# Kernel optimization log

Hardware: AMD Instinct MI355X
Metric: run time of the kernel (lower is better)

The kernel has to match this reference:

```python
import jax, jax.numpy as jnp
import numpy as np
from functools import partial

# CUBA LIF/LI constants (mock-mode software integration, hxtorch conventions)
DT = 1e-6
TAU_MEM_INV = 1.0 / 6e-6   # dt*tau_mem_inv = 1/6 per-step membrane coupling
TAU_SYN_INV = 1.0 / 6e-6   # dt*tau_syn_inv = 1/6 per-step synaptic decay
ALPHA = 50.0               # SuperSpike surrogate steepness
V_TH = 1.0                 # threshold; leak = reset = 0


@partial(jax.custom_vjp, nondiff_argnums=(1,))
def spike_fn(x, alpha):
    # Heaviside forward, SuperSpike surrogate backward.
    return (x > 0.0).astype(x.dtype)

def _spike_fwd(x, alpha):
    return spike_fn(x, alpha), x

def _spike_bwd(alpha, x, g):
    return (g / (alpha * jnp.abs(x) + 1.0) ** 2,)

spike_fn.defvjp(_spike_fwd, _spike_bwd)


def cuba_lif(inp):
    """CUBA LIF integration over time. inp: [T, B, N] synaptic input; returns spikes [T, B, N]."""
    B, N = inp.shape[1], inp.shape[2]
    v0 = jnp.zeros((B, N), inp.dtype)
    i0 = jnp.zeros((B, N), inp.dtype)

    def step(carry, x):
        v, i = carry
        v = v + DT * TAU_MEM_INV * (-v + i)          # membrane update (leak=0)
        i = i * (1.0 - DT * TAU_SYN_INV) + x          # synaptic current decay + input
        z = spike_fn(v - V_TH, ALPHA)                 # spike
        v = (1.0 - jax.lax.stop_gradient(z)) * v      # reset to 0 (detached spike)
        return (v, i), z

    _, z = jax.lax.scan(step, (v0, i0), inp)
    return z


def cuba_li(inp):
    """CUBA LI (non-spiking readout) integration. inp: [T, B, N]; returns membrane trace [T, B, N]."""
    B, N = inp.shape[1], inp.shape[2]
    v0 = jnp.zeros((B, N), inp.dtype)
    i0 = jnp.zeros((B, N), inp.dtype)

    def step(carry, x):
        v, i = carry
        v = v + DT * TAU_MEM_INV * (-v + i)
        i = i * (1.0 - DT * TAU_SYN_INV) + x
        return (v, i), v

    _, v = jax.lax.scan(step, (v0, i0), inp)
    return v


def setup_inputs() -> dict:
    key = jax.random.key(0)
    k1, k2, k3 = jax.random.split(key, 3)
    T, B, N_IN, N_HID, N_OUT = 256, 128, 784, 512, 128
    spikes = (jax.random.uniform(k1, (T, B, N_IN)) < 0.1).astype(jnp.float32)
    w_hidden = 0.2 * jax.random.normal(k2, (N_HID, N_IN), dtype=jnp.float32)
    w_out = 0.2 * jax.random.normal(k3, (N_OUT, N_HID), dtype=jnp.float32)
    return {"spikes": spikes, "w_hidden": w_hidden, "w_out": w_out}


def reference(spikes, w_hidden, w_out):
    # input_repetitions=1 -> repeat is a no-op. Synapses have no bias.
    c_h = jnp.einsum('tbi,hi->tbh', spikes, w_hidden)   # [T, B, n_hidden]
    s_h = cuba_lif(c_h)                                  # hidden spikes
    c_o = jnp.einsum('tbh,oh->tbo', s_h, w_out)          # [T, B, n_out]
    return cuba_li(c_o)                                  # readout membrane trace (v_cadc)
```

## Files before the change

kernel.cpp:

```cpp
#include <hip/hip_runtime.h>

typedef _Float16 f16;
typedef _Float16 f16x8 __attribute__((ext_vector_type(8)));
typedef float f32x4 __attribute__((ext_vector_type(4)));

#define GLOBAL_AS __attribute__((address_space(1)))
#define LDS_AS __attribute__((address_space(3)))

__device__ __forceinline__ void async16(const void* g, void* l) {
  __builtin_amdgcn_global_load_lds((const GLOBAL_AS unsigned int*)g,
                                   (LDS_AS unsigned int*)l, 16, 0, 0);
}

__global__ __launch_bounds__(256) void conv_all(const float* __restrict__ s,
                                                const float* __restrict__ wh,
                                                f16* __restrict__ a16,
                                                f16* __restrict__ w2h) {
  if (blockIdx.x < 12800) {
    int idx = blockIdx.x * 256 + threadIdx.x;
    int m = idx / 100;
    int g = idx - m * 100;
    f16x8 h = {};
    if (g < 98) {
      const float4* p = (const float4*)(s + (size_t)m * 784 + g * 8);
      float4 x = p[0];
      float4 y = p[1];
      h[0] = (f16)x.x; h[1] = (f16)x.y; h[2] = (f16)x.z; h[3] = (f16)x.w;
      h[4] = (f16)y.x; h[5] = (f16)y.y; h[6] = (f16)y.z; h[7] = (f16)y.w;
    }
    *(f16x8*)(a16 + (size_t)m * 800 + g * 8) = h;
  } else {
    int idx = (blockIdx.x - 12800) * 256 + threadIdx.x;
    if (idx < 819200) {
      int h = idx / 1600;
      int c = idx - h * 1600;
      f16 o = (f16)0.f;
      if (c < 784) {
        o = (f16)wh[h * 784 + c];
      } else if (c >= 800 && c < 1584) {
        float x = wh[h * 784 + (c - 800)];
        f16 hi = (f16)x;
        o = (f16)((x - (float)hi) * 2048.0f);
      }
      w2h[idx] = o;
    }
  }
}

template <typename OUT, int N_LD, int A_STRIDE, int B_STRIDE, int NCH64,
          bool TAIL32, int B_OFF_LO, int KSPLIT_SPAN, bool XCD_SWZ>
__global__ __launch_bounds__(256, 2) void gemm_f16(const f16* __restrict__ A,
                                                   const f16* __restrict__ B,
                                                   OUT* __restrict__ C) {
  constexpr bool HAS_LO = (B_OFF_LO > 0);
  __shared__ __align__(16) f16 lds_a[128 * 64];
  __shared__ __align__(16) f16 lds_bh[128 * 64];
  __shared__ __align__(16) f16 lds_bl[HAS_LO ? 128 * 64 : 8];
  const int t = threadIdx.x;
  const int lane = t & 63;
  const int wave = t >> 6;
  int bx, by;
  if (XCD_SWZ) {
    const int b = blockIdx.x;
    by = (b & 7) + 8 * (b >> 5);
    bx = (b >> 3) & 3;
  } else {
    bx = blockIdx.x;
    by = blockIdx.y;
  }
  const int m0 = by * 128;
  const int n0 = KSPLIT_SPAN ? 0 : bx * 128;
  const int kb = KSPLIT_SPAN ? bx * KSPLIT_SPAN : 0;
  OUT* Cp = KSPLIT_SPAN ? C + (size_t)bx * 32768 * N_LD : C;
  const int wm = (wave >> 1) * 64;
  const int wn = (wave & 1) * 64;
  const int row = lane & 15;
  const int quad = lane >> 4;

  f32x4 acch[4][4] = {};
  f32x4 accl[HAS_LO ? 4 : 1][4] = {};

  for (int c = 0; c < NCH64; ++c) {
    const int k0 = kb + c * 64;
#pragma unroll
    for (int s = 0; s < 4; ++s) {
      const int j = t + s * 256;
      const int r = j >> 3;
      const int g = (j & 7) ^ (r & 7);
      async16(A + (m0 + r) * A_STRIDE + k0 + g * 8, &lds_a[j * 8]);
      async16(B + (n0 + r) * B_STRIDE + k0 + g * 8, &lds_bh[j * 8]);
      if (HAS_LO)
        async16(B + (n0 + r) * B_STRIDE + B_OFF_LO + k0 + g * 8, &lds_bl[j * 8]);
    }
    __syncthreads();
#pragma unroll
    for (int ks = 0; ks < 2; ++ks) {
      f16x8 af[4], bh[4], bl[4];
#pragma unroll
      for (int tm = 0; tm < 4; ++tm) {
        const int ra = wm + tm * 16 + row;
        const int p = (ks * 4 + quad) ^ (ra & 7);
        af[tm] = *(const f16x8*)&lds_a[ra * 64 + p * 8];
      }
#pragma unroll
      for (int tn = 0; tn < 4; ++tn) {
        const int rb = wn + tn * 16 + row;
        const int p = (ks * 4 + quad) ^ (rb & 7);
        bh[tn] = *(const f16x8*)&lds_bh[rb * 64 + p * 8];
        if (HAS_LO) bl[tn] = *(const f16x8*)&lds_bl[rb * 64 + p * 8];
      }
#pragma unroll
      for (int tm = 0; tm < 4; ++tm)
#pragma unroll
        for (int tn = 0; tn < 4; ++tn) {
          acch[tm][tn] =
              __builtin_amdgcn_mfma_f32_16x16x32_f16(af[tm], bh[tn], acch[tm][tn], 0, 0, 0);
          if (HAS_LO)
            accl[tm][tn] =
                __builtin_amdgcn_mfma_f32_16x16x32_f16(af[tm], bl[tn], accl[tm][tn], 0, 0, 0);
        }
    }
    __syncthreads();
  }

  if (TAIL32) {
    const int k0 = kb + NCH64 * 64;
#pragma unroll
    for (int s = 0; s < 2; ++s) {
      const int j = t + s * 256;
      const int r = j >> 2;
      const int g = (j & 3) ^ (r & 3);
      async16(A + (m0 + r) * A_STRIDE + k0 + g * 8, &lds_a[j * 8]);
      async16(B + (n0 + r) * B_STRIDE + k0 + g * 8, &lds_bh[j * 8]);
      if (HAS_LO)
        async16(B + (n0 + r) * B_STRIDE + B_OFF_LO + k0 + g * 8, &lds_bl[j * 8]);
    }
    __syncthreads();
    f16x8 af[4], bh[4], bl[4];
#pragma unroll
    for (int tm = 0; tm < 4; ++tm) {
      const int ra = wm + tm * 16 + row;
      const int p = quad ^ (ra & 3);
      af[tm] = *(const f16x8*)&lds_a[ra * 32 + p * 8];
    }
#pragma unroll
    for (int tn = 0; tn < 4; ++tn) {
      const int rb = wn + tn * 16 + row;
      const int p = quad ^ (rb & 3);
      bh[tn] = *(const f16x8*)&lds_bh[rb * 32 + p * 8];
      if (HAS_LO) bl[tn] = *(const f16x8*)&lds_bl[rb * 32 + p * 8];
    }
#pragma unroll
    for (int tm = 0; tm < 4; ++tm)
#pragma unroll
      for (int tn = 0; tn < 4; ++tn) {
        acch[tm][tn] =
            __builtin_amdgcn_mfma_f32_16x16x32_f16(af[tm], bh[tn], acch[tm][tn], 0, 0, 0);
        if (HAS_LO)
          accl[tm][tn] =
              __builtin_amdgcn_mfma_f32_16x16x32_f16(af[tm], bl[tn], accl[tm][tn], 0, 0, 0);
      }
  }

#pragma unroll
  for (int tm = 0; tm < 4; ++tm)
#pragma unroll
    for (int tn = 0; tn < 4; ++tn)
#pragma unroll
      for (int r = 0; r < 4; ++r) {
        const int mm = m0 + wm + tm * 16 + quad * 4 + r;
        const int nn = n0 + wn + tn * 16 + row;
        float val = acch[tm][tn][r];
        if (HAS_LO) val += 4.8828125e-4f * accl[tm][tn][r];
        Cp[(size_t)mm * N_LD + nn] = (OUT)val;
      }
}

__global__ __launch_bounds__(512, 2) void fused_bgl(const f16* __restrict__ ch,
                                                    const float* __restrict__ wo,
                                                    float* __restrict__ out) {
  const int b = blockIdx.x;
  const int tid = threadIdx.x;
  const int lane = tid & 63;
  const int wave = tid >> 6;
  const int trow = lane & 15;
  const int quad = lane >> 4;

  __shared__ __align__(16) f16 s_lds[32 * 512];
  __shared__ __align__(16) float co_lds[32][132];

  f16x8 bfrag[16];
  {
    const float* wp = wo + (wave * 16 + trow) * 512 + quad * 8;
#pragma unroll
    for (int ks = 0; ks < 16; ++ks) {
      const float4* p = (const float4*)(wp + ks * 32);
      float4 x = p[0];
      float4 y = p[1];
      f16x8 hh;
      hh[0] = (f16)x.x; hh[1] = (f16)x.y; hh[2] = (f16)x.z; hh[3] = (f16)x.w;
      hh[4] = (f16)y.x; hh[5] = (f16)y.y; hh[6] = (f16)y.z; hh[7] = (f16)y.w;
      bfrag[ks] = hh;
    }
  }

  const int h = tid;
  float v = 0.f, cur = 0.f;
  float lv = 0.f, lcur = 0.f;

  f16 xa[32], xb[32];
#pragma unroll
  for (int j = 0; j < 32; ++j) xa[j] = ch[((size_t)(j * 128 + b)) * 512 + h];

  for (int c = 0; c < 8; ++c) {
    if (c < 7) {
#pragma unroll
      for (int j = 0; j < 32; ++j)
        xb[j] = ch[((size_t)(((c + 1) * 32 + j) * 128 + b)) * 512 + h];
    }
#pragma unroll
    for (int j = 0; j < 32; ++j) {
      float x = (float)xa[j];
      v = v + 0.16666667f * (cur - v);
      cur = 0.8333333f * cur + x;
      bool z = v > 1.0f;
      v = z ? 0.f : v;
      s_lds[j * 512 + (((h >> 3) ^ (j & 7)) << 3) + (h & 7)] = z ? (f16)1.f : (f16)0.f;
    }
#pragma unroll
    for (int j = 0; j < 32; ++j) xa[j] = xb[j];
    __syncthreads();

    f32x4 acc0 = {};
    f32x4 acc1 = {};
#pragma unroll
    for (int ks = 0; ks < 16; ++ks) {
      const int G = ks * 4 + quad;
      f16x8 a0 = *(const f16x8*)&s_lds[trow * 512 + ((G ^ (trow & 7)) << 3)];
      f16x8 a1 = *(const f16x8*)&s_lds[(16 + trow) * 512 + ((G ^ (trow & 7)) << 3)];
      acc0 = __builtin_amdgcn_mfma_f32_16x16x32_f16(a0, bfrag[ks], acc0, 0, 0, 0);
      acc1 = __builtin_amdgcn_mfma_f32_16x16x32_f16(a1, bfrag[ks], acc1, 0, 0, 0);
    }
#pragma unroll
    for (int r = 0; r < 4; ++r) {
      co_lds[quad * 4 + r][wave * 16 + trow] = acc0[r];
      co_lds[16 + quad * 4 + r][wave * 16 + trow] = acc1[r];
    }
    __syncthreads();

    if (tid < 128) {
#pragma unroll
      for (int j = 0; j < 32; ++j) {
        float x = co_lds[j][tid];
        lv = lv + 0.16666667f * (lcur - lv);
        lcur = 0.8333333f * lcur + x;
        out[((size_t)((c * 32 + j) * 128 + b)) * 128 + tid] = lv;
      }
    }
  }
}

extern "C" void kernel_launch(void* const* d_in, const int* in_sizes, int n_in,
                              void* d_out, int out_size, void* d_ws, size_t ws_size,
                              hipStream_t stream) {
  const float* spikes = (const float*)d_in[0];
  const float* w_hidden = (const float*)d_in[1];
  const float* w_out = (const float*)d_in[2];
  float* out = (float*)d_out;

  char* ws = (char*)d_ws;
  f16* A16 = (f16*)ws;
  f16* w2h = (f16*)(ws + 52428800);
  f16* c_h = (f16*)(ws + 52428800 + 1638400);

  conv_all<<<16000, 256, 0, stream>>>(spikes, w_hidden, A16, w2h);

  gemm_f16<f16, 512, 800, 1600, 12, true, 800, 0, true>
      <<<1024, 256, 0, stream>>>(A16, w2h, c_h);

  fused_bgl<<<128, 512, 0, stream>>>(c_h, w_out, out);
}
```

Before: 239.3 us.

## Double-buffer GEMM1 LDS loads with async prefetch of next K chunk

Replaces the templated single-buffered GEMM with a specialized kernel that stages K in 32-wide chunks into two LDS buffers. It prefetches the next chunk with global_load_lds while computing the current one, using vmcnt waits and raw barriers. The aim is to hide global-load latency behind MFMA work. In exchange, the K step per barrier halves, so twice as many barriers run. The last iteration also issues a redundant reload of chunk 24.

```diff
diff --git a/kernel.cpp b/kernel.cpp
--- a/kernel.cpp
+++ b/kernel.cpp
@@ -47,108 +47,67 @@
   }
 }
 
-template <typename OUT, int N_LD, int A_STRIDE, int B_STRIDE, int NCH64,
-          bool TAIL32, int B_OFF_LO, int KSPLIT_SPAN, bool XCD_SWZ>
-__global__ __launch_bounds__(256, 2) void gemm_f16(const f16* __restrict__ A,
-                                                   const f16* __restrict__ B,
-                                                   OUT* __restrict__ C) {
-  constexpr bool HAS_LO = (B_OFF_LO > 0);
-  __shared__ __align__(16) f16 lds_a[128 * 64];
-  __shared__ __align__(16) f16 lds_bh[128 * 64];
-  __shared__ __align__(16) f16 lds_bl[HAS_LO ? 128 * 64 : 8];
+__global__ __launch_bounds__(256, 2) void gemm1_pipe(const f16* __restrict__ A,
+                                                     const f16* __restrict__ B,
+                                                     f16* __restrict__ C) {
+  __shared__ __align__(16) f16 lds_a[2][128 * 32];
+  __shared__ __align__(16) f16 lds_bh[2][128 * 32];
+  __shared__ __align__(16) f16 lds_bl[2][128 * 32];
   const int t = threadIdx.x;
   const int lane = t & 63;
   const int wave = t >> 6;
-  int bx, by;
-  if (XCD_SWZ) {
-    const int b = blockIdx.x;
-    by = (b & 7) + 8 * (b >> 5);
-    bx = (b >> 3) & 3;
-  } else {
-    bx = blockIdx.x;
-    by = blockIdx.y;
-  }
+  const int b = blockIdx.x;
+  const int by = (b & 7) + 8 * (b >> 5);
+  const int bx = (b >> 3) & 3;
   const int m0 = by * 128;
-  const int n0 = KSPLIT_SPAN ? 0 : bx * 128;
-  const int kb = KSPLIT_SPAN ? bx * KSPLIT_SPAN : 0;
-  OUT* Cp = KSPLIT_SPAN ? C + (size_t)bx * 32768 * N_LD : C;
+  const int n0 = bx * 128;
   const int wm = (wave >> 1) * 64;
   const int wn = (wave & 1) * 64;
   const int row = lane & 15;
   const int quad = lane >> 4;
 
+  const int j0 = t, j1 = t + 256;
+  const int r0 = j0 >> 2, g0 = (j0 & 3) ^ (r0 & 3);
+  const int r1 = j1 >> 2, g1 = (j1 & 3) ^ (r1 & 3);
+
   f32x4 acch[4][4] = {};
-  f32x4 accl[HAS_LO ? 4 : 1][4] = {};
-
-  for (int c = 0; c < NCH64; ++c) {
-    const int k0 = kb + c * 64;
-#pragma unroll
-    for (int s = 0; s < 4; ++s) {
-      const int j = t + s * 256;
-      const int r = j >> 3;
-      const int g = (j & 7) ^ (r & 7);
-      async16(A + (m0 + r) * A_STRIDE + k0 + g * 8, &lds_a[j * 8]);
-      async16(B + (n0 + r) * B_STRIDE + k0 + g * 8, &lds_bh[j * 8]);
-      if (HAS_LO)
-        async16(B + (n0 + r) * B_STRIDE + B_OFF_LO + k0 + g * 8, &lds_bl[j * 8]);
-    }
-    __syncthreads();
-#pragma unroll
-    for (int ks = 0; ks < 2; ++ks) {
-      f16x8 af[4], bh[4], bl[4];
-#pragma unroll
-      for (int tm = 0; tm < 4; ++tm) {
-        const int ra = wm + tm * 16 + row;
-        const int p = (ks * 4 + quad) ^ (ra & 7);
-        af[tm] = *(const f16x8*)&lds_a[ra * 64 + p * 8];
-      }
-#pragma unroll
-      for (int tn = 0; tn < 4; ++tn) {
-        const int rb = wn + tn * 16 + row;
-        const int p = (ks * 4 + quad) ^ (rb & 7);
-        bh[tn] = *(const f16x8*)&lds_bh[rb * 64 + p * 8];
-        if (HAS_LO) bl[tn] = *(const f16x8*)&lds_bl[rb * 64 + p * 8];
-      }
-#pragma unroll
-      for (int tm = 0; tm < 4; ++tm)
-#pragma unroll
-        for (int tn = 0; tn < 4; ++tn) {
-          acch[tm][tn] =
-              __builtin_amdgcn_mfma_f32_16x16x32_f16(af[tm], bh[tn], acch[tm][tn], 0, 0, 0);
-          if (HAS_LO)
-            accl[tm][tn] =
-                __builtin_amdgcn_mfma_f32_16x16x32_f16(af[tm], bl[tn], accl[tm][tn], 0, 0, 0);
-        }
-    }
-    __syncthreads();
-  }
-
-  if (TAIL32) {
-    const int k0 = kb + NCH64 * 64;
-#pragma unroll
-    for (int s = 0; s < 2; ++s) {
-      const int j = t + s * 256;
-      const int r = j >> 2;
-      const int g = (j & 3) ^ (r & 3);
-      async16(A + (m0 + r) * A_STRIDE + k0 + g * 8, &lds_a[j * 8]);
-      async16(B + (n0 + r) * B_STRIDE + k0 + g * 8, &lds_bh[j * 8]);
-      if (HAS_LO)
-        async16(B + (n0 + r) * B_STRIDE + B_OFF_LO + k0 + g * 8, &lds_bl[j * 8]);
-    }
-    __syncthreads();
+  f32x4 accl[4][4] = {};
+
+#define STAGE1(c, bi)                                                   \
+  {                                                                     \
+    const int k0 = (c) * 32;                                            \
+    async16(A + (m0 + r0) * 800 + k0 + g0 * 8, &lds_a[bi][j0 * 8]);     \
+    async16(A + (m0 + r1) * 800 + k0 + g1 * 8, &lds_a[bi][j1 * 8]);     \
+    async16(B + (n0 + r0) * 1600 + k0 + g0 * 8, &lds_bh[bi][j0 * 8]);   \
+    async16(B + (n0 + r1) * 1600 + k0 + g1 * 8, &lds_bh[bi][j1 * 8]);   \
+    async16(B + (n0 + r0) * 1600 + 800 + k0 + g0 * 8, &lds_bl[bi][j0 * 8]); \
+    async16(B + (n0 + r1) * 1600 + 800 + k0 + g1 * 8, &lds_bl[bi][j1 * 8]); \
+  }
+
+  STAGE1(0, 0);
+  for (int c = 0; c < 25; ++c) {
+    __builtin_amdgcn_s_barrier();
+    const int cn = (c + 1 < 25) ? c + 1 : 24;
+    STAGE1(cn, (c + 1) & 1);
+    asm volatile("s_waitcnt vmcnt(6)" ::: "memory");
+    __builtin_amdgcn_sched_barrier(0);
+    __builtin_amdgcn_s_barrier();
+    const f16* la = lds_a[c & 1];
+    const f16* lbh = lds_bh[c & 1];
+    const f16* lbl = lds_bl[c & 1];
     f16x8 af[4], bh[4], bl[4];
 #pragma unroll
     for (int tm = 0; tm < 4; ++tm) {
       const int ra = wm + tm * 16 + row;
       const int p = quad ^ (ra & 3);
-      af[tm] = *(const f16x8*)&lds_a[ra * 32 + p * 8];
+      af[tm] = *(const f16x8*)&la[ra * 32 + p * 8];
     }
 #pragma unroll
     for (int tn = 0; tn < 4; ++tn) {
       const int rb = wn + tn * 16 + row;
       const int p = quad ^ (rb & 3);
-      bh[tn] = *(const f16x8*)&lds_bh[rb * 32 + p * 8];
-      if (HAS_LO) bl[tn] = *(const f16x8*)&lds_bl[rb * 32 + p * 8];
+      bh[tn] = *(const f16x8*)&lbh[rb * 32 + p * 8];
+      bl[tn] = *(const f16x8*)&lbl[rb * 32 + p * 8];
     }
 #pragma unroll
     for (int tm = 0; tm < 4; ++tm)
@@ -156,11 +115,11 @@
       for (int tn = 0; tn < 4; ++tn) {
         acch[tm][tn] =
             __builtin_amdgcn_mfma_f32_16x16x32_f16(af[tm], bh[tn], acch[tm][tn], 0, 0, 0);
-        if (HAS_LO)
-          accl[tm][tn] =
-              __builtin_amdgcn_mfma_f32_16x16x32_f16(af[tm], bl[tn], accl[tm][tn], 0, 0, 0);
-      }
-  }
+        accl[tm][tn] =
+            __builtin_amdgcn_mfma_f32_16x16x32_f16(af[tm], bl[tn], accl[tm][tn], 0, 0, 0);
+      }
+  }
+#undef STAGE1
 
 #pragma unroll
   for (int tm = 0; tm < 4; ++tm)
@@ -170,9 +129,7 @@
       for (int r = 0; r < 4; ++r) {
         const int mm = m0 + wm + tm * 16 + quad * 4 + r;
         const int nn = n0 + wn + tn * 16 + row;
-        float val = acch[tm][tn][r];
-        if (HAS_LO) val += 4.8828125e-4f * accl[tm][tn][r];
-        Cp[(size_t)mm * N_LD + nn] = (OUT)val;
+        C[(size_t)mm * 512 + nn] = (f16)(acch[tm][tn][r] + 4.8828125e-4f * accl[tm][tn][r]);
       }
 }
 
@@ -275,8 +232,7 @@
 
   conv_all<<<16000, 256, 0, stream>>>(spikes, w_hidden, A16, w2h);
 
-  gemm_f16<f16, 512, 800, 1600, 12, true, 800, 0, true>
-      <<<1024, 256, 0, stream>>>(A16, w2h, c_h);
+  gemm1_pipe<<<1024, 256, 0, stream>>>(A16, w2h, c_h);
 
   fused_bgl<<<128, 512, 0, stream>>>(c_h, w_out, out);
 }
```

Result: slower. 251.7 us (+5.2%).
